# Kernel optimization log

Measured on AMD Instinct MI355X. Metric: run time of the kernel, lower is better.

Reference implementation:

```python
import jax, jax.numpy as jnp
import numpy as np

N_NODES = 50000
N_HOPS = 4
N_EDGES = 800000
NFEAT = 512
HIDDEN = 512
NCLASS = 128
ATT_HID = 64


def setup_inputs() -> dict:
    key = jax.random.key(0)
    ks = jax.random.split(key, 12)
    s = lambda *sh: 1.0 / np.sqrt(sh[0])
    inp = {}
    inp['x'] = jax.random.normal(ks[0], (N_NODES, NFEAT), dtype=jnp.float32)
    inp['W1'] = jax.random.normal(ks[1], (NFEAT, HIDDEN), dtype=jnp.float32) * s(NFEAT)
    inp['W2'] = jax.random.normal(ks[2], (HIDDEN, NCLASS), dtype=jnp.float32) * s(HIDDEN)
    inp['b2'] = jax.random.normal(ks[3], (NCLASS,), dtype=jnp.float32) * 0.01
    inp['Wg'] = jax.random.normal(ks[4], (NCLASS, NCLASS), dtype=jnp.float32) * s(NCLASS)
    inp['Wa'] = jax.random.normal(ks[5], (2 * NCLASS, ATT_HID), dtype=jnp.float32) * s(2 * NCLASS)
    inp['ba'] = jax.random.normal(ks[6], (ATT_HID,), dtype=jnp.float32) * 0.01
    inp['va'] = jax.random.normal(ks[7], (ATT_HID,), dtype=jnp.float32) * s(ATT_HID)
    inp['adj_values'] = jax.random.uniform(ks[8], (N_HOPS, N_EDGES), dtype=jnp.float32)
    inp['adj_indices'] = jax.random.randint(ks[9], (N_HOPS, 2, N_EDGES), 0, N_NODES, dtype=jnp.int32)
    inp['idx'] = jnp.arange(N_NODES, dtype=jnp.int32)
    return inp


def reference(x, W1, W2, b2, Wg, Wa, ba, va, adj_values, adj_indices, idx):
    # x: [N, nfeat] -> relu(linear1) -> linear2 : [N, C]
    z = jax.nn.relu(x @ W1) @ W2 + b2  # [N, C]
    anchor = z[idx]                    # [Na, C]
    na = idx.shape[0]
    n_hops = adj_indices.shape[0]
    embs = [anchor]
    for h in range(n_hops):  # fixed small structural loop over hops
        rows = adj_indices[h, 0]  # destination anchor row per edge
        cols = adj_indices[h, 1]  # source node per edge
        # sparse matmul: agg[r] = sum_e v_e * z[cols_e]  (LayerConvol)
        agg = jax.ops.segment_sum(adj_values[h][:, None] * z[cols], rows, num_segments=na)
        embs.append(agg @ Wg)  # [Na, C]
    seq = jnp.stack(embs, axis=1)  # [Na, H+1, C]
    # AttenMlp: additive attention of anchor query over hop embeddings
    q = jnp.broadcast_to(anchor[:, None, :], seq.shape)       # [Na, H+1, C]
    feat = jnp.concatenate([q, seq], axis=-1)                 # [Na, H+1, 2C]
    scores = jnp.tanh(feat @ Wa + ba) @ va                    # [Na, H+1]
    alpha = jax.nn.softmax(scores, axis=1)
    out = jnp.einsum('nh,nhc->nc', alpha, seq)                # [Na, C]
    return jax.nn.log_softmax(out, axis=1)
```

## Files before the change

### kernel.cpp

```cpp
#include <hip/hip_runtime.h>

#define NA    50000
#define NFEAT 512
#define HID   512
#define NC    128
#define AH    64
#define NE    800000
#define NHOP  4
#define NBUCK 196
#define CAPB  5120

typedef __bf16 bf16x8 __attribute__((ext_vector_type(8)));
typedef float  f32x4  __attribute__((ext_vector_type(4)));

__device__ __forceinline__ unsigned short f2bf(float f){
  union { float f; unsigned u; } a; a.f = f;
  return (unsigned short)((a.u + 0x7fffu + ((a.u >> 16) & 1u)) >> 16);
}
__device__ __forceinline__ float bf2f(unsigned short h){
  union { unsigned u; float f; } a; a.u = ((unsigned)h) << 16;
  return a.f;
}
__device__ __forceinline__ float uasf(unsigned u){
  union { unsigned u; float f; } a; a.u = u;
  return a.f;
}
__device__ __forceinline__ float tanh_fast(float x){
  x = fminf(15.f, fmaxf(-15.f, x));
  float e = __expf(2.f * x);
  return (e - 1.f) / (e + 1.f);
}

__device__ __forceinline__ void g2l16(const void* g, void* l){
  __builtin_amdgcn_global_load_lds(
      (const __attribute__((address_space(1))) void*)g,
      (__attribute__((address_space(3))) void*)l, 16, 0, 0);
}


__global__ void cast_x_kernel(const float* __restrict__ in, unsigned short* __restrict__ out, int n4){
  int i = blockIdx.x * 256 + threadIdx.x;
  if (i >= n4) return;
  float4 v = reinterpret_cast<const float4*>(in)[i];
  ushort4 o; o.x = f2bf(v.x); o.y = f2bf(v.y); o.z = f2bf(v.z); o.w = f2bf(v.w);
  reinterpret_cast<ushort4*>(out)[i] = o;
}

__global__ void transpose_cast_kernel(const float* __restrict__ in, unsigned short* __restrict__ out,
                                      int R, int N){
  int i = blockIdx.x * 256 + threadIdx.x;
  if (i >= R * N) return;
  int n = i / R, k = i - n * R;
  out[i] = f2bf(in[(size_t)k * N + n]);
}

__global__ void build_wa_kernel(const float* __restrict__ Wa, unsigned short* __restrict__ WaT){
  int i = blockIdx.x * 256 + threadIdx.x;
  if (i >= 128 * 128) return;
  int n = i >> 7, k = i & 127;
  float v = (n < 64) ? Wa[(size_t)k * AH + n] : Wa[(size_t)(128 + k) * AH + (n - 64)];
  WaT[i] = f2bf(v);
}

__global__ void wfuse_kernel(const float* __restrict__ Wa, const float* __restrict__ Wg,
                             unsigned short* __restrict__ WfuseT){
  int i = blockIdx.x * 256 + threadIdx.x;
  if (i >= 64 * 128) return;
  int j = i >> 7, n = i & 127;
  float s = 0.f;
  for (int k = 0; k < 128; k++)
    s += Wa[(size_t)(128 + k) * AH + j] * Wg[(size_t)n * 128 + k];
  WfuseT[i] = f2bf(s);
}

template<int OP, int SWZ>
__global__ __launch_bounds__(256) void gemm_bt(
    const unsigned short* __restrict__ A, const unsigned short* __restrict__ BT,
    float* __restrict__ Cf, unsigned short* __restrict__ Cb,
    const float* __restrict__ bias,
    int M, int N, int K)
{
  int row0, col0;
  if (SWZ){
    const int xcd = blockIdx.x & 7, slot = blockIdx.x >> 3;
    const int r = xcd * 49 + (slot >> 2);
    if (r >= 391) return;
    row0 = r * 128; col0 = (slot & 3) * 128;
  } else {
    row0 = blockIdx.x * 128; col0 = blockIdx.y * 128;
  }
  __shared__ unsigned short As[128 * 32];
  __shared__ unsigned short Bs[128 * 32];
  const int tid = threadIdx.x;
  const int wave = tid >> 6, lane = tid & 63;
  const int wr = (wave >> 1) * 64, wc = (wave & 1) * 64;
  f32x4 acc[4][4];
  #pragma unroll
  for (int m = 0; m < 4; m++)
    #pragma unroll
    for (int n = 0; n < 4; n++) acc[m][n] = (f32x4){0.f, 0.f, 0.f, 0.f};
  const int lrow = lane >> 2, lk = (lane & 3) * 8;

  for (int k0 = 0; k0 < K; k0 += 32){
    __syncthreads();
    #pragma unroll
    for (int j = 0; j < 2; j++){
      const int rb = (wave * 2 + j) * 16;
      const int ra = rb + lrow;
      int gr = row0 + ra; gr = gr < M ? gr : M - 1;
      g2l16(A + (size_t)gr * K + k0 + lk, As + rb * 32);
      int gc = col0 + ra; gc = gc < N ? gc : N - 1;
      g2l16(BT + (size_t)gc * K + k0 + lk, Bs + rb * 32);
    }
    __syncthreads();
    bf16x8 af[4], bfr[4];
    #pragma unroll
    for (int m = 0; m < 4; m++)
      af[m] = *reinterpret_cast<const bf16x8*>(&As[(wr + m * 16 + (lane & 15)) * 32 + (lane >> 4) * 8]);
    #pragma unroll
    for (int n = 0; n < 4; n++)
      bfr[n] = *reinterpret_cast<const bf16x8*>(&Bs[(wc + n * 16 + (lane & 15)) * 32 + (lane >> 4) * 8]);
    #pragma unroll
    for (int m = 0; m < 4; m++)
      #pragma unroll
      for (int n = 0; n < 4; n++)
        acc[m][n] = __builtin_amdgcn_mfma_f32_16x16x32_bf16(af[m], bfr[n], acc[m][n], 0, 0, 0);
  }

  const int rbase = row0 + wr + (lane >> 4) * 4;
  const int cbase = col0 + wc + (lane & 15);
  #pragma unroll
  for (int m = 0; m < 4; m++){
    #pragma unroll
    for (int n = 0; n < 4; n++){
      const int col = cbase + n * 16;
      #pragma unroll
      for (int i = 0; i < 4; i++){
        const int row = rbase + m * 16 + i;
        if (row < M && col < N){
          float v = acc[m][n][i];
          if (OP == 0){ v = v > 0.f ? v : 0.f; Cb[(size_t)row * N + col] = f2bf(v); }
          else {
            v += bias[col];
            Cf[(size_t)row * N + col] = v;
            Cb[(size_t)row * N + col] = f2bf(v);
          }
        }
      }
    }
  }
}

__global__ __launch_bounds__(256) void gemm_sweep(
    const unsigned short* __restrict__ aggbf, const unsigned short* __restrict__ zbf,
    const unsigned short* __restrict__ WgT, const unsigned short* __restrict__ WfuseT,
    const unsigned short* __restrict__ WaT,
    unsigned short* __restrict__ embs, unsigned short* __restrict__ EW, float* __restrict__ ZW)
{
  const int zi = blockIdx.z;
  const unsigned short* A; const unsigned short* BT;
  unsigned short* Cb = nullptr; float* Cf = nullptr; int N;
  if (zi < 4)      { A = aggbf + (size_t)zi * NA * NC;       BT = WgT;    Cb = embs + (size_t)zi * NA * NC; N = 128; }
  else if (zi < 8) { A = aggbf + (size_t)(zi - 4) * NA * NC; BT = WfuseT; Cb = EW + (size_t)(zi - 4) * NA * AH; N = 64; }
  else             { A = zbf;                                BT = WaT;    Cf = ZW; N = 128; }

  __shared__ unsigned short As[128 * 32];
  __shared__ unsigned short Bs[128 * 32];
  const int tid = threadIdx.x;
  const int wave = tid >> 6, lane = tid & 63;
  const int row0 = blockIdx.x * 128;
  const int wr = (wave >> 1) * 64, wc = (wave & 1) * 64;
  f32x4 acc[4][4];
  #pragma unroll
  for (int m = 0; m < 4; m++)
    #pragma unroll
    for (int n = 0; n < 4; n++) acc[m][n] = (f32x4){0.f, 0.f, 0.f, 0.f};

  for (int k0 = 0; k0 < 128; k0 += 32){
    __syncthreads();
    #pragma unroll
    for (int j = 0; j < 2; j++){
      const int rb = (wave * 2 + j) * 16;
      int gr = row0 + rb + (lane >> 2); gr = gr < NA ? gr : NA - 1;
      g2l16(A + (size_t)gr * 128 + k0 + (lane & 3) * 8, As + rb * 32);
      int gc = rb + (lane >> 2); gc = gc < N ? gc : N - 1;
      g2l16(BT + (size_t)gc * 128 + k0 + (lane & 3) * 8, Bs + rb * 32);
    }
    __syncthreads();
    bf16x8 bfr[4];
    #pragma unroll
    for (int n = 0; n < 4; n++)
      bfr[n] = *reinterpret_cast<const bf16x8*>(&Bs[(wc + n * 16 + (lane & 15)) * 32 + (lane >> 4) * 8]);
    #pragma unroll
    for (int m = 0; m < 4; m++){
      bf16x8 a = *reinterpret_cast<const bf16x8*>(&As[(wr + m * 16 + (lane & 15)) * 32 + (lane >> 4) * 8]);
      #pragma unroll
      for (int n = 0; n < 4; n++)
        acc[m][n] = __builtin_amdgcn_mfma_f32_16x16x32_bf16(a, bfr[n], acc[m][n], 0, 0, 0);
    }
  }

  const int rbase = row0 + wr + (lane >> 4) * 4;
  const int cbase = wc + (lane & 15);
  #pragma unroll
  for (int m = 0; m < 4; m++){
    #pragma unroll
    for (int n = 0; n < 4; n++){
      const int col = cbase + n * 16;
      #pragma unroll
      for (int i = 0; i < 4; i++){
        const int row = rbase + m * 16 + i;
        if (row < NA && col < N){
          float v = acc[m][n][i];
          if (Cf) Cf[(size_t)row * N + col] = v;
          else    Cb[(size_t)row * N + col] = f2bf(v);
        }
      }
    }
  }
}

__global__ __launch_bounds__(256) void binA_kernel(
    const int* __restrict__ adji, const float* __restrict__ adjv,
    int* __restrict__ fill, long long* __restrict__ binned)
{
  const int h = blockIdx.y, tid = threadIdx.x;
  const int e0 = blockIdx.x * 2048;
  __shared__ int lhist[NBUCK], lbase[NBUCK], lfill[NBUCK];
  for (int i = tid; i < NBUCK; i += 256){ lhist[i] = 0; lfill[i] = 0; }
  __syncthreads();
  int rr[8]; unsigned hh[8]; float vv[8];
  #pragma unroll
  for (int k = 0; k < 8; k++){
    int e = e0 + k * 256 + tid;
    bool ok = e < NE;
    int r = ok ? adji[(size_t)h * 2 * NE + e] : -1;
    int c = ok ? adji[(size_t)h * 2 * NE + NE + e] : 0;
    vv[k] = ok ? adjv[(size_t)h * NE + e] : 0.f;
    rr[k] = r;
    hh[k] = ((unsigned)(r & 255) << 17) | (unsigned)c;
    if (ok) atomicAdd(&lhist[r >> 8], 1);
  }
  __syncthreads();
  if (tid < NBUCK) lbase[tid] = atomicAdd(&fill[h * NBUCK + tid], lhist[tid]);
  __syncthreads();
  #pragma unroll
  for (int k = 0; k < 8; k++){
    if (rr[k] >= 0){
      int b = rr[k] >> 8;
      int p = lbase[b] + atomicAdd(&lfill[b], 1);
      if (p < CAPB)
        binned[((size_t)(h * NBUCK + b)) * CAPB + p] =
            ((long long)hh[k] << 32) | (unsigned)__float_as_int(vv[k]);
    }
  }
}

__global__ __launch_bounds__(1024) void bscan_kernel(const int* __restrict__ fill,
                                                     int* __restrict__ bbase, int* __restrict__ offs){
  __shared__ int tmp[1024];
  int tid = threadIdx.x;
  int v = (tid < NHOP * NBUCK) ? fill[tid] : 0;
  tmp[tid] = v; __syncthreads();
  for (int o = 1; o < 1024; o <<= 1){
    int t = (tid >= o) ? tmp[tid - o] : 0;
    __syncthreads();
    tmp[tid] += t;
    __syncthreads();
  }
  if (tid < NHOP * NBUCK) bbase[tid] = tmp[tid] - v;
  if (tid == 0) offs[NHOP * NA] = NHOP * NE;
}

__global__ __launch_bounds__(256) void binB_kernel(
    const int* __restrict__ fill, const int* __restrict__ bbase,
    const long long* __restrict__ binned,
    int* __restrict__ offs, long long* __restrict__ pvc)
{
  const int b = blockIdx.x, h = blockIdx.y, tid = threadIdx.x;
  const int hb = h * NBUCK + b;
  const int cnt = min(fill[hb], CAPB);
  const long long* src = binned + (size_t)hb * CAPB;
  const int gbase = bbase[hb];
  const int rowbase = b << 8;
  const int nrows = min(256, NA - rowbase);
  __shared__ long long sdata[CAPB];
  __shared__ int lhist[256], lpre[256], lfill2[256];
  lhist[tid] = 0; lfill2[tid] = 0;
  __syncthreads();
  for (int p = tid; p < cnt; p += 256)
    atomicAdd(&lhist[(unsigned)(src[p] >> 32) >> 17], 1);
  __syncthreads();
  int v = lhist[tid]; lpre[tid] = v; __syncthreads();
  for (int o = 1; o < 256; o <<= 1){
    int t = (tid >= o) ? lpre[tid - o] : 0;
    __syncthreads();
    lpre[tid] += t;
    __syncthreads();
  }
  int excl = lpre[tid] - v;
  if (tid < nrows) offs[h * NA + rowbase + tid] = gbase + excl;
  lpre[tid] = excl;
  __syncthreads();
  for (int p = tid; p < cnt; p += 256){
    long long rec = src[p];
    unsigned hi = (unsigned)(rec >> 32);
    int lr = hi >> 17;
    long long out = (rec & 0xffffffffLL) | ((long long)(hi & 0x1ffffu) << 32);
    int pos = lpre[lr] + atomicAdd(&lfill2[lr], 1);
    if (pos < CAPB) sdata[pos] = out;
    else            pvc[(size_t)gbase + pos] = out;
  }
  __syncthreads();
  for (int p = tid; p < cnt; p += 256)
    pvc[(size_t)gbase + p] = sdata[p];
}

#define GR 4
__global__ __launch_bounds__(256) void gather_kernel(
    const int* __restrict__ offs, const long long* __restrict__ pvc,
    const unsigned short* __restrict__ zbf, unsigned short* __restrict__ aggbf)
{
  const int h = blockIdx.y;
  const int w = threadIdx.x >> 6, lane = threadIdx.x & 63;
  const int row = blockIdx.x * GR + w;
  const int base = h * NA + row;
  const int s = offs[base], e = offs[base + 1];
  __shared__ alignas(16) long long srec[GR][64];
  const unsigned* z32 = (const unsigned*)zbf;
  const int4* sr2 = (const int4*)&srec[w][0];
  float a0 = 0.f, a1 = 0.f, b0 = 0.f, b1 = 0.f;
  for (int p0 = s; p0 < e; p0 += 64){
    long long r = 0;
    if (p0 + lane < e) r = __builtin_nontemporal_load(&pvc[p0 + lane]);
    srec[w][lane] = r;
    const int quads = (min(64, e - p0) + 3) >> 2;
    #pragma unroll 2
    for (int q = 0; q < quads; q++){
      int4 ra = sr2[2 * q], rb = sr2[2 * q + 1];
      unsigned z0 = z32[((unsigned)ra.y << 6) + lane];
      unsigned z1 = z32[((unsigned)ra.w << 6) + lane];
      unsigned z2 = z32[((unsigned)rb.y << 6) + lane];
      unsigned z3 = z32[((unsigned)rb.w << 6) + lane];
      float v0 = uasf((unsigned)ra.x), v1 = uasf((unsigned)ra.z);
      float v2 = uasf((unsigned)rb.x), v3 = uasf((unsigned)rb.z);
      a0 += v0 * uasf(z0 << 16); a1 += v0 * uasf(z0 & 0xffff0000u);
      b0 += v1 * uasf(z1 << 16); b1 += v1 * uasf(z1 & 0xffff0000u);
      a0 += v2 * uasf(z2 << 16); a1 += v2 * uasf(z2 & 0xffff0000u);
      b0 += v3 * uasf(z3 << 16); b1 += v3 * uasf(z3 & 0xffff0000u);
    }
  }
  ushort2 o; o.x = f2bf(a0 + b0); o.y = f2bf(a1 + b1);
  *reinterpret_cast<ushort2*>(aggbf + (size_t)base * NC + lane * 2) = o;
}

__global__ __launch_bounds__(256) void final_kernel(
    const float* __restrict__ z, const unsigned short* __restrict__ embs,
    const float* __restrict__ ZW, const unsigned short* __restrict__ EW,
    const float* __restrict__ ba, const float* __restrict__ va,
    const int* __restrict__ idx, float* __restrict__ out)
{
  int tid = threadIdx.x, wave = tid >> 6, lane = tid & 63;
  int n = blockIdx.x * 4 + wave;
  if (n >= NA) return;
  int an = idx[n];
  float qa = ZW[(size_t)an * NC + lane] + ba[lane];
  float vaj = va[lane];
  float sc[5];
  {
    float s0 = ZW[(size_t)an * NC + 64 + lane];
    float t = tanh_fast(qa + s0) * vaj;
    #pragma unroll
    for (int o = 32; o; o >>= 1) t += __shfl_xor(t, o);
    sc[0] = t;
  }
  #pragma unroll
  for (int h = 1; h < 5; h++){
    float sh = bf2f(EW[((size_t)(h - 1) * NA + n) * AH + lane]);
    float t = tanh_fast(qa + sh) * vaj;
    #pragma unroll
    for (int o = 32; o; o >>= 1) t += __shfl_xor(t, o);
    sc[h] = t;
  }
  float m = sc[0];
  #pragma unroll
  for (int h = 1; h < 5; h++) m = fmaxf(m, sc[h]);
  float al[5], den = 0.f;
  #pragma unroll
  for (int h = 0; h < 5; h++){ al[h] = __expf(sc[h] - m); den += al[h]; }
  float inv = 1.f / den;
  float o0 = al[0] * z[(size_t)an * NC + lane];
  float o1 = al[0] * z[(size_t)an * NC + 64 + lane];
  #pragma unroll
  for (int h = 1; h < 5; h++){
    o0 += al[h] * bf2f(embs[((size_t)(h - 1) * NA + n) * NC + lane]);
    o1 += al[h] * bf2f(embs[((size_t)(h - 1) * NA + n) * NC + 64 + lane]);
  }
  o0 *= inv; o1 *= inv;
  float mx = fmaxf(o0, o1);
  #pragma unroll
  for (int o = 32; o; o >>= 1) mx = fmaxf(mx, __shfl_xor(mx, o));
  float se = __expf(o0 - mx) + __expf(o1 - mx);
  #pragma unroll
  for (int o = 32; o; o >>= 1) se += __shfl_xor(se, o);
  float ls = __logf(se);
  out[(size_t)n * NC + lane]      = o0 - mx - ls;
  out[(size_t)n * NC + 64 + lane] = o1 - mx - ls;
}


extern "C" void kernel_launch(void* const* d_in, const int* in_sizes, int n_in,
                              void* d_out, int out_size, void* d_ws, size_t ws_size,
                              hipStream_t stream)
{
  const float* x    = (const float*)d_in[0];
  const float* W1   = (const float*)d_in[1];
  const float* W2   = (const float*)d_in[2];
  const float* b2   = (const float*)d_in[3];
  const float* Wg   = (const float*)d_in[4];
  const float* Wa   = (const float*)d_in[5];
  const float* ba   = (const float*)d_in[6];
  const float* va   = (const float*)d_in[7];
  const float* adjv = (const float*)d_in[8];
  const int*   adji = (const int*)d_in[9];
  const int*   idx  = (const int*)d_in[10];
  float* out = (float*)d_out;
  (void)in_sizes; (void)n_in; (void)out_size; (void)ws_size;

  char* w = (char*)d_ws;
  auto alloc = [&](size_t b) -> char* { char* p = w; w += (b + 255) & ~(size_t)255; return p; };
  unsigned short* Scr1 = (unsigned short*)alloc((size_t)NA * NFEAT * 2);
  unsigned short* Hbuf = (unsigned short*)alloc((size_t)NA * HID * 2);
  unsigned short* W1T  = (unsigned short*)alloc((size_t)HID * NFEAT * 2);
  unsigned short* W2T  = (unsigned short*)alloc((size_t)NC * HID * 2);
  unsigned short* WgT  = (unsigned short*)alloc((size_t)NC * NC * 2);
  unsigned short* WaT  = (unsigned short*)alloc((size_t)NC * NC * 2);
  unsigned short* WfuseT = (unsigned short*)alloc((size_t)AH * NC * 2);
  float*          z    = (float*)alloc((size_t)NA * NC * 4);
  unsigned short* zbf  = (unsigned short*)alloc((size_t)NA * NC * 2);
  float*          ZW   = (float*)alloc((size_t)NA * NC * 4);
  int* fill  = (int*)alloc((size_t)NHOP * NBUCK * 4);
  int* bbase = (int*)alloc((size_t)NHOP * NBUCK * 4);
  int* offs  = (int*)alloc(((size_t)NHOP * NA + 1) * 4);
  long long* pvc = (long long*)alloc((size_t)NHOP * NE * 8);
  unsigned short* Xbf   = Scr1;
  long long* binned     = (long long*)Scr1;
  unsigned short* embs  = Scr1;
  unsigned short* aggbf = Hbuf;
  unsigned short* EW    = (unsigned short*)pvc;

  cast_x_kernel<<<dim3((NA * NFEAT / 4 + 255) / 256), 256, 0, stream>>>(x, Xbf, NA * NFEAT / 4);
  transpose_cast_kernel<<<dim3((NFEAT * HID + 255) / 256), 256, 0, stream>>>(W1, W1T, NFEAT, HID);
  transpose_cast_kernel<<<dim3((HID * NC + 255) / 256), 256, 0, stream>>>(W2, W2T, HID, NC);
  transpose_cast_kernel<<<dim3((NC * NC + 255) / 256), 256, 0, stream>>>(Wg, WgT, NC, NC);
  build_wa_kernel<<<dim3(64), 256, 0, stream>>>(Wa, WaT);
  wfuse_kernel<<<dim3(32), 256, 0, stream>>>(Wa, Wg, WfuseT);

  gemm_bt<0, 1><<<dim3(1568, 1, 1), 256, 0, stream>>>(Xbf, W1T, nullptr, Hbuf, nullptr, NA, HID, NFEAT);
  gemm_bt<1, 0><<<dim3(391, 1, 1), 256, 0, stream>>>(Hbuf, W2T, z, zbf, b2, NA, NC, HID);

  hipMemsetAsync(fill, 0, (size_t)NHOP * NBUCK * 4, stream);
  binA_kernel<<<dim3((NE + 2047) / 2048, NHOP), 256, 0, stream>>>(adji, adjv, fill, binned);
  bscan_kernel<<<dim3(1), 1024, 0, stream>>>(fill, bbase, offs);
  binB_kernel<<<dim3(NBUCK, NHOP), 256, 0, stream>>>(fill, bbase, binned, offs, pvc);

  gather_kernel<<<dim3(NA / GR, NHOP), 256, 0, stream>>>(offs, pvc, zbf, aggbf);
  gemm_sweep<<<dim3(391, 1, 9), 256, 0, stream>>>(aggbf, zbf, WgT, WfuseT, WaT, embs, EW, ZW);

  final_kernel<<<dim3(NA / 4), 256, 0, stream>>>(z, embs, ZW, EW, ba, va, idx, out);
}
```

Baseline: 353.0 us.

## Merge weight prep kernels, drop fp32 z copy, unroll gather loop further

Five small weight transpose/cast kernels are merged into one prep kernel dispatched by block range, which removes launch overhead. The second GEMM no longer writes an fp32 copy of z. The final kernel reads the bf16 z instead, which saves about 25MB of writes and some reads but lowers the precision of the anchor term. The gather loop unroll goes from 2 to 4 to expose more outstanding loads.

New measurement: 341.2 us. -3.4%, faster.

```diff
diff --git a/kernel.cpp b/kernel.cpp
--- a/kernel.cpp
+++ b/kernel.cpp
@@ -46,38 +46,43 @@
   reinterpret_cast<ushort4*>(out)[i] = o;
 }
 
-__global__ void transpose_cast_kernel(const float* __restrict__ in, unsigned short* __restrict__ out,
-                                      int R, int N){
-  int i = blockIdx.x * 256 + threadIdx.x;
-  if (i >= R * N) return;
-  int n = i / R, k = i - n * R;
-  out[i] = f2bf(in[(size_t)k * N + n]);
-}
-
-__global__ void build_wa_kernel(const float* __restrict__ Wa, unsigned short* __restrict__ WaT){
-  int i = blockIdx.x * 256 + threadIdx.x;
-  if (i >= 128 * 128) return;
-  int n = i >> 7, k = i & 127;
-  float v = (n < 64) ? Wa[(size_t)k * AH + n] : Wa[(size_t)(128 + k) * AH + (n - 64)];
-  WaT[i] = f2bf(v);
-}
-
-__global__ void wfuse_kernel(const float* __restrict__ Wa, const float* __restrict__ Wg,
-                             unsigned short* __restrict__ WfuseT){
-  int i = blockIdx.x * 256 + threadIdx.x;
-  if (i >= 64 * 128) return;
-  int j = i >> 7, n = i & 127;
-  float s = 0.f;
-  for (int k = 0; k < 128; k++)
-    s += Wa[(size_t)(128 + k) * AH + j] * Wg[(size_t)n * 128 + k];
-  WfuseT[i] = f2bf(s);
+__global__ void prep_kernel(const float* __restrict__ W1, const float* __restrict__ W2,
+                            const float* __restrict__ Wg, const float* __restrict__ Wa,
+                            unsigned short* __restrict__ W1T, unsigned short* __restrict__ W2T,
+                            unsigned short* __restrict__ WgT, unsigned short* __restrict__ WaT,
+                            unsigned short* __restrict__ WfuseT){
+  const int b = blockIdx.x, tid = threadIdx.x;
+  if (b < 1024){
+    int i = b * 256 + tid;
+    int n = i >> 9, k = i & 511;
+    W1T[i] = f2bf(W1[(size_t)k * HID + n]);
+  } else if (b < 1280){
+    int i = (b - 1024) * 256 + tid;
+    int n = i >> 9, k = i & 511;
+    W2T[i] = f2bf(W2[(size_t)k * NC + n]);
+  } else if (b < 1344){
+    int i = (b - 1280) * 256 + tid;
+    int n = i >> 7, k = i & 127;
+    WgT[i] = f2bf(Wg[(size_t)k * NC + n]);
+  } else if (b < 1408){
+    int i = (b - 1344) * 256 + tid;
+    int n = i >> 7, k = i & 127;
+    float v = (n < 64) ? Wa[(size_t)k * AH + n] : Wa[(size_t)(128 + k) * AH + (n - 64)];
+    WaT[i] = f2bf(v);
+  } else {
+    int i = (b - 1408) * 256 + tid;
+    int j = i >> 7, n = i & 127;
+    float s = 0.f;
+    for (int k = 0; k < 128; k++)
+      s += Wa[(size_t)(128 + k) * AH + j] * Wg[(size_t)n * 128 + k];
+    WfuseT[i] = f2bf(s);
+  }
 }
 
 template<int OP, int SWZ>
 __global__ __launch_bounds__(256) void gemm_bt(
     const unsigned short* __restrict__ A, const unsigned short* __restrict__ BT,
-    float* __restrict__ Cf, unsigned short* __restrict__ Cb,
-    const float* __restrict__ bias,
+    unsigned short* __restrict__ Cb, const float* __restrict__ bias,
     int M, int N, int K)
 {
   int row0, col0;
@@ -139,12 +144,9 @@
         const int row = rbase + m * 16 + i;
         if (row < M && col < N){
           float v = acc[m][n][i];
-          if (OP == 0){ v = v > 0.f ? v : 0.f; Cb[(size_t)row * N + col] = f2bf(v); }
-          else {
-            v += bias[col];
-            Cf[(size_t)row * N + col] = v;
-            Cb[(size_t)row * N + col] = f2bf(v);
-          }
+          if (OP == 0){ v = v > 0.f ? v : 0.f; }
+          else        { v += bias[col]; }
+          Cb[(size_t)row * N + col] = f2bf(v);
         }
       }
     }
@@ -335,7 +337,7 @@
     if (p0 + lane < e) r = __builtin_nontemporal_load(&pvc[p0 + lane]);
     srec[w][lane] = r;
     const int quads = (min(64, e - p0) + 3) >> 2;
-    #pragma unroll 2
+    #pragma unroll 4
     for (int q = 0; q < quads; q++){
       int4 ra = sr2[2 * q], rb = sr2[2 * q + 1];
       unsigned z0 = z32[((unsigned)ra.y << 6) + lane];
@@ -355,7 +357,7 @@
 }
 
 __global__ __launch_bounds__(256) void final_kernel(
-    const float* __restrict__ z, const unsigned short* __restrict__ embs,
+    const unsigned short* __restrict__ zbf, const unsigned short* __restrict__ embs,
     const float* __restrict__ ZW, const unsigned short* __restrict__ EW,
     const float* __restrict__ ba, const float* __restrict__ va,
     const int* __restrict__ idx, float* __restrict__ out)
@@ -389,8 +391,8 @@
   #pragma unroll
   for (int h = 0; h < 5; h++){ al[h] = __expf(sc[h] - m); den += al[h]; }
   float inv = 1.f / den;
-  float o0 = al[0] * z[(size_t)an * NC + lane];
-  float o1 = al[0] * z[(size_t)an * NC + 64 + lane];
+  float o0 = al[0] * bf2f(zbf[(size_t)an * NC + lane]);
+  float o1 = al[0] * bf2f(zbf[(size_t)an * NC + 64 + lane]);
   #pragma unroll
   for (int h = 1; h < 5; h++){
     o0 += al[h] * bf2f(embs[((size_t)(h - 1) * NA + n) * NC + lane]);
@@ -436,7 +438,6 @@
   unsigned short* WgT  = (unsigned short*)alloc((size_t)NC * NC * 2);
   unsigned short* WaT  = (unsigned short*)alloc((size_t)NC * NC * 2);
   unsigned short* WfuseT = (unsigned short*)alloc((size_t)AH * NC * 2);
-  float*          z    = (float*)alloc((size_t)NA * NC * 4);
   unsigned short* zbf  = (unsigned short*)alloc((size_t)NA * NC * 2);
   float*          ZW   = (float*)alloc((size_t)NA * NC * 4);
   int* fill  = (int*)alloc((size_t)NHOP * NBUCK * 4);
@@ -450,14 +451,10 @@
   unsigned short* EW    = (unsigned short*)pvc;
 
   cast_x_kernel<<<dim3((NA * NFEAT / 4 + 255) / 256), 256, 0, stream>>>(x, Xbf, NA * NFEAT / 4);
-  transpose_cast_kernel<<<dim3((NFEAT * HID + 255) / 256), 256, 0, stream>>>(W1, W1T, NFEAT, HID);
-  transpose_cast_kernel<<<dim3((HID * NC + 255) / 256), 256, 0, stream>>>(W2, W2T, HID, NC);
-  transpose_cast_kernel<<<dim3((NC * NC + 255) / 256), 256, 0, stream>>>(Wg, WgT, NC, NC);
-  build_wa_kernel<<<dim3(64), 256, 0, stream>>>(Wa, WaT);
-  wfuse_kernel<<<dim3(32), 256, 0, stream>>>(Wa, Wg, WfuseT);
-
-  gemm_bt<0, 1><<<dim3(1568, 1, 1), 256, 0, stream>>>(Xbf, W1T, nullptr, Hbuf, nullptr, NA, HID, NFEAT);
-  gemm_bt<1, 0><<<dim3(391, 1, 1), 256, 0, stream>>>(Hbuf, W2T, z, zbf, b2, NA, NC, HID);
+  prep_kernel<<<dim3(1440), 256, 0, stream>>>(W1, W2, Wg, Wa, W1T, W2T, WgT, WaT, WfuseT);
+
+  gemm_bt<0, 1><<<dim3(1568, 1, 1), 256, 0, stream>>>(Xbf, W1T, Hbuf, nullptr, NA, HID, NFEAT);
+  gemm_bt<1, 0><<<dim3(391, 1, 1), 256, 0, stream>>>(Hbuf, W2T, zbf, b2, NA, NC, HID);
 
   hipMemsetAsync(fill, 0, (size_t)NHOP * NBUCK * 4, stream);
   binA_kernel<<<dim3((NE + 2047) / 2048, NHOP), 256, 0, stream>>>(adji, adjv, fill, binned);
@@ -467,5 +464,5 @@
   gather_kernel<<<dim3(NA / GR, NHOP), 256, 0, stream>>>(offs, pvc, zbf, aggbf);
   gemm_sweep<<<dim3(391, 1, 9), 256, 0, stream>>>(aggbf, zbf, WgT, WfuseT, WaT, embs, EW, ZW);
 
-  final_kernel<<<dim3(NA / 4), 256, 0, stream>>>(z, embs, ZW, EW, ba, va, idx, out);
-}
+  final_kernel<<<dim3(NA / 4), 256, 0, stream>>>(zbf, embs, ZW, EW, ba, va, idx, out);
+}
```
